# Kernel tuning notes

Hardware: AMD Instinct MI355X
Metric: run time of the kernel (lower is better)

The kernel has to match this reference:

```python
import jax, jax.numpy as jnp
import numpy as np

B, N = 4096, 12
HID = 64
SLOPE = 0.2   # GATv2Conv default negative_slope
ALPHA = 0.1   # skip-connection scale


def _gabriel_adjacency(p):
    # p: [B, N, 2] node positions. Gabriel graph: edge (i,j) iff no other
    # point k lies inside the closed disk with diameter segment (p_i, p_j).
    n = p.shape[1]
    mid = (p[:, :, None, :] + p[:, None, :, :]) * 0.5                      # [B,N,N,2]
    r2 = jnp.sum((p[:, :, None, :] - p[:, None, :, :]) ** 2, -1) * 0.25    # [B,N,N]
    d2 = jnp.sum((p[:, None, None, :, :] - mid[:, :, :, None, :]) ** 2, -1)  # [B,i,j,k]
    eye = jnp.eye(n, dtype=bool)
    excl = eye[:, None, :] | eye[None, :, :]                               # k==i or k==j
    d2 = jnp.where(excl[None], jnp.inf, d2)
    gab = jnp.all(d2 > r2[..., None], axis=-1) & (~eye)[None]
    # undirected edges + self loops (GATv2Conv add_self_loops=True default)
    return gab | jnp.swapaxes(gab, 1, 2) | eye[None]                       # [B,N,N]


def _gatv2(x, adj, wl, wr, att, b):
    # PyG GATv2Conv, heads=1: e_ij = att . leaky_relu(W_l x_j + W_r x_i),
    # alpha = softmax_j(e_ij) over neighbors, out_i = sum_j alpha_ij W_l x_j + b.
    xl = x @ wl                                                            # source feats [B,N,H]
    xr = x @ wr                                                            # target feats [B,N,H]
    s = jax.nn.leaky_relu(xl[:, None, :, :] + xr[:, :, None, :], SLOPE)    # [B,i,j,H]
    e = jnp.einsum('bijh,h->bij', s, att)
    e = jnp.where(adj, e, -1e9)
    a = jax.nn.softmax(e, axis=-1)                                         # over sources j
    return jnp.einsum('bij,bjh->bih', a, xl) + b


def _forward(batch, enc_w1, enc_b1, enc_w2, enc_b2, enc_w3, enc_b3,
             g1_wl, g1_wr, g1_att, g1_b, g2_wl, g2_wr, g2_att, g2_b,
             g3_wl, g3_wr, g3_att, g3_b, g4_wl, g4_wr, g4_att, g4_b,
             lab_w, lab_b, val_w, val_b, skip_w, skip_b):
    h = jax.nn.relu(batch @ enc_w1 + enc_b1)
    h = jax.nn.relu(h @ enc_w2 + enc_b2)
    latent = h @ enc_w3 + enc_b3                                           # [B,N,3]
    # graph construction is non-differentiable (scipy in the original)
    adj = _gabriel_adjacency(jax.lax.stop_gradient(latent[..., :2]))
    x0 = latent[..., 2:3]                                                  # [B,N,1]
    x1 = jax.nn.relu(_gatv2(x0, adj, g1_wl, g1_wr, g1_att, g1_b))
    x2 = jax.nn.relu(_gatv2(x1, adj, g2_wl, g2_wr, g2_att, g2_b))
    skip = latent @ skip_w + skip_b
    x3 = jax.nn.relu(_gatv2(x2, adj, g3_wl, g3_wr, g3_att, g3_b) + ALPHA * skip)
    logits = x3 @ lab_w + lab_b                                            # [B,N,4]
    # note: original feeds x2 (not x3) into gcn4 -- kept faithful
    x4 = jax.nn.relu(_gatv2(x2, adj, g4_wl, g4_wr, g4_att, g4_b) + ALPHA * skip)
    values = x4 @ val_w + val_b                                            # [B,N,1]
    return batch[:, :, :4], batch[:, :, 4:5], logits, values, latent


def setup_inputs():
    key = jax.random.key(0)
    ks = iter(jax.random.split(key, 40))
    def rnd(shape, s=0.1):
        return jax.random.normal(next(ks), shape, dtype=jnp.float32) * s
    inp = {"batch": jax.random.normal(next(ks), (B, N, 5), dtype=jnp.float32)}
    inp.update(enc_w1=rnd((5, HID)), enc_b1=jnp.zeros((HID,), jnp.float32),
               enc_w2=rnd((HID, HID)), enc_b2=jnp.zeros((HID,), jnp.float32),
               enc_w3=rnd((HID, 3)), enc_b3=jnp.zeros((3,), jnp.float32))
    for i, cin in zip((1, 2, 3, 4), (1, HID, HID, HID)):
        inp[f"g{i}_wl"] = rnd((cin, HID)); inp[f"g{i}_wr"] = rnd((cin, HID))
        inp[f"g{i}_att"] = rnd((HID,)); inp[f"g{i}_b"] = jnp.zeros((HID,), jnp.float32)
    inp.update(lab_w=rnd((HID, 4)), lab_b=jnp.zeros((4,), jnp.float32),
               val_w=rnd((HID, 1)), val_b=jnp.zeros((1,), jnp.float32),
               skip_w=rnd((3, HID)), skip_b=jnp.zeros((HID,), jnp.float32))
    return inp


def reference(batch, enc_w1, enc_b1, enc_w2, enc_b2, enc_w3, enc_b3,
              g1_wl, g1_wr, g1_att, g1_b, g2_wl, g2_wr, g2_att, g2_b,
              g3_wl, g3_wr, g3_att, g3_b, g4_wl, g4_wr, g4_att, g4_b,
              lab_w, lab_b, val_w, val_b, skip_w, skip_b):
    return _forward(batch, enc_w1, enc_b1, enc_w2, enc_b2, enc_w3, enc_b3,
                    g1_wl, g1_wr, g1_att, g1_b, g2_wl, g2_wr, g2_att, g2_b,
                    g3_wl, g3_wr, g3_att, g3_b, g4_wl, g4_wr, g4_att, g4_b,
                    lab_w, lab_b, val_w, val_b, skip_w, skip_b)
```

## Files before the change

kernel.cpp:

```cpp
#include <hip/hip_runtime.h>
#include <hip/hip_bf16.h>
#include <math.h>

#define N     12
#define HID   64
#define STP   68
#define XST   72
#define SLOPE 0.2f
#define ALPHA 0.1f

typedef float v2f __attribute__((ext_vector_type(2)));
typedef float v4f __attribute__((ext_vector_type(4)));
typedef int   i4  __attribute__((ext_vector_type(4)));
typedef short v8s __attribute__((ext_vector_type(8)));

static __device__ __forceinline__ v8s as_v8s(i4 v) {
    union { i4 a; v8s b; } u; u.a = v; return u.b;
}

#define OUT0 0
#define OUT1 196608
#define OUT2 245760
#define OUT3 442368
#define OUT4 491520

__global__ void prep_kernel(const float* __restrict__ enc_w2,
                            const float* __restrict__ g2_wl, const float* __restrict__ g2_wr,
                            const float* __restrict__ g3_wl, const float* __restrict__ g3_wr,
                            const float* __restrict__ g4_wl, const float* __restrict__ g4_wr,
                            const float* __restrict__ lab_w,
                            float* __restrict__ ws) {
    int t = threadIdx.x;
    int bx = blockIdx.x;
    if (bx < 64) {
        int c = bx;
        ws[t*64 + c] = enc_w2[c*64 + t];
        return;
    }
    if (bx == 112) {
        #pragma unroll
        for (int c = 0; c < 4; c++) ws[16384 + c*64 + t] = lab_w[t*4 + c];
        return;
    }
    int idx = bx - 64;
    int mat = idx >> 3, rem = idx & 7;
    int kt = rem >> 2, nt = rem & 3;
    const float* src;
    switch (mat) {
        case 0: src = g2_wl; break;
        case 1: src = g2_wr; break;
        case 2: src = g3_wl; break;
        case 3: src = g3_wr; break;
        case 4: src = g4_wl; break;
        default: src = g4_wr; break;
    }
    int quad = t >> 4, col = t & 15;
    int n = nt*16 + col;
    unsigned* dst = (unsigned*)(ws + 4096) + mat*2048 + (kt*4+nt)*256 + t*4;
    #pragma unroll
    for (int jp = 0; jp < 4; jp++) {
        int k0 = kt*32 + quad*8 + 2*jp;
        __hip_bfloat16 h0 = __float2bfloat16(src[(k0+0)*64 + n]);
        __hip_bfloat16 h1 = __float2bfloat16(src[(k0+1)*64 + n]);
        unsigned u0 = *(unsigned short*)&h0, u1 = *(unsigned short*)&h1;
        dst[jp] = u0 | (u1 << 16);
    }
}

template<bool TW>
__global__ __launch_bounds__(64, 3) void gae_kernel(
    const float* __restrict__ batch,
    const float* __restrict__ enc_w1, const float* __restrict__ enc_b1,
    const float* __restrict__ enc_w2, const float* __restrict__ enc_b2,
    const float* __restrict__ enc_w3, const float* __restrict__ enc_b3,
    const float* __restrict__ g1_wl, const float* __restrict__ g1_wr,
    const float* __restrict__ g1_att, const float* __restrict__ g1_b,
    const float* __restrict__ g2_wl, const float* __restrict__ g2_wr,
    const float* __restrict__ g2_att, const float* __restrict__ g2_b,
    const float* __restrict__ g3_wl, const float* __restrict__ g3_wr,
    const float* __restrict__ g3_att, const float* __restrict__ g3_b,
    const float* __restrict__ g4_wl, const float* __restrict__ g4_wr,
    const float* __restrict__ g4_att, const float* __restrict__ g4_b,
    const float* __restrict__ lab_w, const float* __restrict__ lab_b,
    const float* __restrict__ val_w, const float* __restrict__ val_b,
    const float* __restrict__ skip_w, const float* __restrict__ skip_b,
    const float* __restrict__ wsT,
    float* __restrict__ out)
{
    const int b = blockIdx.x;
    const int t = threadIdx.x;

    __shared__ __align__(16) float bufL[N*STP];
    __shared__ __align__(16) float bufR[N*STP];
    __shared__ __align__(16) unsigned short xB16[N*XST];
    __shared__ __align__(16) float pool[144];
    __shared__ __align__(16) float att_s[HID];
    __shared__ __align__(16) unsigned char pairs8[64];

    const v2f z2 = {0.f, 0.f};
    const v4f z4 = {0.f, 0.f, 0.f, 0.f};
    const v4f s4 = {SLOPE, SLOPE, SLOPE, SLOPE};

    const int p0 = t,        i0 = p0 / N, j0 = p0 - i0*N;
    const int p1 = t + 64,   i1 = p1 / N, j1 = p1 - i1*N;
    const int p2 = (t < 16) ? (t + 128) : 143;
    const int i2 = p2 / N,   j2 = p2 - i2*N;

    if (t < N*5) {
        float v = batch[b*(N*5) + t];
        pool[t] = v;
        int i = t / 5, f = t - i*5;
        if (f < 4) out[OUT0 + (size_t)b*(N*4) + i*4 + f] = v;
        else       out[OUT1 + (size_t)b*N + i] = v;
    }
    __syncthreads();

    {
        float acc[N];
        float bias = enc_b1[t];
        #pragma unroll
        for (int i=0;i<N;i++) acc[i] = bias;
        #pragma unroll
        for (int f=0; f<5; f++) {
            float w = enc_w1[f*HID + t];
            #pragma unroll
            for (int i=0;i<N;i++) acc[i] = fmaf(pool[i*5+f], w, acc[i]);
        }
        #pragma unroll
        for (int i=0;i<N;i++) bufL[i*STP + t] = fmaxf(acc[i], 0.f);
    }
    __syncthreads();

    {
        v2f acc[N];
        #pragma unroll
        for (int i=0;i<N;i++) acc[i] = z2;
        const float* w2p = TW ? (wsT + t*HID) : nullptr;
        for (int c=0;c<HID;c+=4) {
            v2f w01, w23;
            if (TW) {
                v4f w4 = *reinterpret_cast<const v4f*>(&w2p[c]);
                w01 = w4.xy; w23 = w4.zw;
            } else {
                w01 = (v2f){enc_w2[(c+0)*HID+t], enc_w2[(c+1)*HID+t]};
                w23 = (v2f){enc_w2[(c+2)*HID+t], enc_w2[(c+3)*HID+t]};
            }
            #pragma unroll
            for (int i=0;i<N;i++) {
                v4f xv = *reinterpret_cast<const v4f*>(&bufL[i*STP + c]);
                acc[i] = __builtin_elementwise_fma(xv.xy, w01, acc[i]);
                acc[i] = __builtin_elementwise_fma(xv.zw, w23, acc[i]);
            }
        }
        float bias = enc_b2[t];
        #pragma unroll
        for (int i=0;i<N;i++) bufR[i*STP + t] = fmaxf(bias + acc[i].x + acc[i].y, 0.f);
    }
    __syncthreads();

    if (t < N*3) {
        int i = t / 3, c = t - i*3;
        float acc = enc_b3[c];
        for (int k=0;k<HID;k+=4) {
            v4f xv = *reinterpret_cast<const v4f*>(&bufR[i*STP + k]);
            acc = fmaf(xv.x, enc_w3[(k+0)*3+c], acc);
            acc = fmaf(xv.y, enc_w3[(k+1)*3+c], acc);
            acc = fmaf(xv.z, enc_w3[(k+2)*3+c], acc);
            acc = fmaf(xv.w, enc_w3[(k+3)*3+c], acc);
        }
        pool[t] = acc;
        out[OUT4 + (size_t)b*(N*3) + t] = acc;
    }
    __syncthreads();

    float skipv[N];
    {
        float w0 = skip_w[t], w1 = skip_w[HID+t], w2 = skip_w[2*HID+t];
        float bias = skip_b[t];
        #pragma unroll
        for (int i=0;i<N;i++) {
            float v = bias;
            v = fmaf(pool[i*3+0], w0, v);
            v = fmaf(pool[i*3+1], w1, v);
            v = fmaf(pool[i*3+2], w2, v);
            skipv[i] = v;
        }
    }

    auto gab = [&](int i, int j)->bool {
        if (i == j) return false;
        float pix = pool[i*3], piy = pool[i*3+1];
        float pjx = pool[j*3], pjy = pool[j*3+1];
        float mx = (pix + pjx) * 0.5f, my = (piy + pjy) * 0.5f;
        float dx = pix - pjx, dy = piy - pjy;
        float r2 = (dx*dx + dy*dy) * 0.25f;
        bool g = true;
        #pragma unroll
        for (int k=0;k<N;k++) {
            float ex = pool[k*3] - mx, ey = pool[k*3+1] - my;
            bool ok = (k == i) || (k == j) || (ex*ex + ey*ey > r2);
            g = g && ok;
        }
        return g;
    };
    unsigned long long gb0 = __ballot(gab(i0, j0));
    unsigned long long gb1 = __ballot(gab(i1, j1));
    unsigned long long gb2 = __ballot((t < 16) && gab(i2, j2));
    auto gbit = [&](int p)->int {
        unsigned long long m = (p < 64) ? gb0 : ((p < 128) ? gb1 : gb2);
        return (int)((m >> (p & 63)) & 1ull);
    };
    const int adjA = gbit(p0) | gbit(j0*N+i0) | (i0 == j0);
    const int adjB = gbit(p1) | gbit(j1*N+i1) | (i1 == j1);
    const int adjC = (t < 16) ? (gbit(p2) | gbit(j2*N+i2) | (i2 == j2)) : 0;

    auto mbcnt64 = [&](unsigned long long m)->int {
        return __builtin_amdgcn_mbcnt_hi((unsigned)(m >> 32),
               __builtin_amdgcn_mbcnt_lo((unsigned)m, 0));
    };
    const unsigned long long am0 = __ballot(adjA != 0);
    const unsigned long long am1 = __ballot(adjB != 0);
    const unsigned long long am2 = __ballot(adjC != 0);
    const int c0  = __popcll(am0);
    const int c01 = c0 + __popcll(am1);
    const int nv  = c01 + __popcll(am2);
    const int idx0 = mbcnt64(am0);
    const int idx1 = c0  + mbcnt64(am1);
    const int idx2 = c01 + mbcnt64(am2);
    if (adjA)               pairs8[idx0] = (unsigned char)p0;
    if (adjB && idx1 < 64)  pairs8[idx1] = (unsigned char)p1;
    if (adjC && idx2 < 64)  pairs8[idx2] = (unsigned char)p2;
    const bool ovB = adjB && (idx1 >= 64);
    const bool ovC = adjC && (idx2 >= 64);
    const int nvc = nv < 64 ? nv : 64;

    auto scoreAt = [&](int i, int j)->float {
        const float* Lj = &bufL[j*STP];
        const float* Ri = &bufR[i*STP];
        v4f a = z4;
        for (int h=0; h<HID; h+=4) {
            v4f a4 = *reinterpret_cast<const v4f*>(&att_s[h]);
            v4f xl = *reinterpret_cast<const v4f*>(Lj + h);
            v4f xr = *reinterpret_cast<const v4f*>(Ri + h);
            v4f s = xl + xr;
            v4f l = __builtin_elementwise_fma(s4, __builtin_elementwise_min(s, z4),
                                              __builtin_elementwise_max(s, z4));
            a = __builtin_elementwise_fma(a4, l, a);
        }
        return (a.x + a.y) + (a.z + a.w);
    };

    auto gat_core = [&](const float* __restrict__ att, const float* __restrict__ gb,
                        int outBf16, int useSkip) {
        att_s[t] = att[t];
        pool[t] = 0.f; pool[t+64] = 0.f;
        if (t < 16) pool[t+128] = 0.f;
        __syncthreads();
        if (t < nvc) {
            int p = pairs8[t];
            int i = (p * 171) >> 11;
            int j = p - i*N;
            pool[p] = __expf(scoreAt(i, j));
        }
        if (nv > 64) {
            if (ovB) pool[p1] = __expf(scoreAt(i1, j1));
            if (ovC) pool[p2] = __expf(scoreAt(i2, j2));
        }
        __syncthreads();
        {
            float xj[N];
            #pragma unroll
            for (int j=0;j<N;j++) xj[j] = bufL[j*STP + t];
            v4f X0 = {xj[0], xj[1], xj[2],  xj[3]};
            v4f X1 = {xj[4], xj[5], xj[6],  xj[7]};
            v4f X2 = {xj[8], xj[9], xj[10], xj[11]};
            float bias = gb[t];
            #pragma unroll
            for (int i=0;i<N;i++) {
                const v4f* ep = reinterpret_cast<const v4f*>(&pool[i*N]);
                v4f e0 = ep[0], e1 = ep[1], e2 = ep[2];
                float sum = ((e0.x+e0.y)+(e0.z+e0.w))
                          + ((e1.x+e1.y)+(e1.z+e1.w))
                          + ((e2.x+e2.y)+(e2.z+e2.w));
                v4f acc = __builtin_elementwise_fma(e0, X0,
                          __builtin_elementwise_fma(e1, X1, e2*X2));
                float r = bias + ((acc.x + acc.y) + (acc.z + acc.w)) / sum;
                if (useSkip) r = fmaf(ALPHA, skipv[i], r);
                r = fmaxf(r, 0.f);
                if (outBf16) {
                    __hip_bfloat16 hv = __float2bfloat16(r);
                    xB16[i*XST + t] = *(unsigned short*)&hv;
                } else {
                    bufR[i*STP + t] = r;
                }
            }
        }
        __syncthreads();
    };

    auto stage_mfma = [&](int matL) {
        const int m = t & 15, quad = t >> 4;
        const int mc = (m < N) ? m : 0;
        i4 aF0 = *reinterpret_cast<const i4*>(&xB16[mc*XST + quad*8]);
        i4 aF1 = *reinterpret_cast<const i4*>(&xB16[mc*XST + 32 + quad*8]);
        const i4* bbase = reinterpret_cast<const i4*>(wsT + 4096);
        #pragma unroll
        for (int mm=0; mm<2; mm++) {
            const i4* bp = bbase + (matL + mm)*512;
            v4f acc[4] = {z4, z4, z4, z4};
            #pragma unroll
            for (int nt=0; nt<4; nt++) {
                i4 b0 = bp[(0*4+nt)*64 + t];
                i4 b1 = bp[(1*4+nt)*64 + t];
                acc[nt] = __builtin_amdgcn_mfma_f32_16x16x32_bf16(as_v8s(aF0), as_v8s(b0), acc[nt], 0, 0, 0);
                acc[nt] = __builtin_amdgcn_mfma_f32_16x16x32_bf16(as_v8s(aF1), as_v8s(b1), acc[nt], 0, 0, 0);
            }
            float* dst = (mm == 0) ? bufL : bufR;
            if (quad < 3) {
                #pragma unroll
                for (int nt=0; nt<4; nt++) {
                    #pragma unroll
                    for (int r=0; r<4; r++)
                        dst[(quad*4+r)*STP + nt*16 + m] = acc[nt][r];
                }
            }
        }
    };

    auto stage = [&](const float* __restrict__ wl, const float* __restrict__ wr) {
        v2f al[N], ar[N];
        #pragma unroll
        for (int i=0;i<N;i++) { al[i] = z2; ar[i] = z2; }
        for (int c=0;c<HID;c+=4) {
            v2f wl01 = (v2f){wl[(c+0)*HID+t], wl[(c+1)*HID+t]};
            v2f wl23 = (v2f){wl[(c+2)*HID+t], wl[(c+3)*HID+t]};
            v2f wr01 = (v2f){wr[(c+0)*HID+t], wr[(c+1)*HID+t]};
            v2f wr23 = (v2f){wr[(c+2)*HID+t], wr[(c+3)*HID+t]};
            #pragma unroll
            for (int i=0;i<N;i++) {
                const unsigned short* xp = &xB16[i*XST + c];
                v4f xv = { __uint_as_float((unsigned)xp[0] << 16),
                           __uint_as_float((unsigned)xp[1] << 16),
                           __uint_as_float((unsigned)xp[2] << 16),
                           __uint_as_float((unsigned)xp[3] << 16) };
                al[i] = __builtin_elementwise_fma(xv.xy, wl01, al[i]);
                al[i] = __builtin_elementwise_fma(xv.zw, wl23, al[i]);
                ar[i] = __builtin_elementwise_fma(xv.xy, wr01, ar[i]);
                ar[i] = __builtin_elementwise_fma(xv.zw, wr23, ar[i]);
            }
        }
        #pragma unroll
        for (int i=0;i<N;i++) {
            bufL[i*STP + t] = al[i].x + al[i].y;
            bufR[i*STP + t] = ar[i].x + ar[i].y;
        }
    };

    {
        float wlv = g1_wl[t], wrv = g1_wr[t];
        #pragma unroll
        for (int i=0;i<N;i++) {
            float v = pool[i*3+2];
            bufL[i*STP + t] = v * wlv;
            bufR[i*STP + t] = v * wrv;
        }
    }
    gat_core(g1_att, g1_b, 1, 0);

    if (TW) stage_mfma(0); else stage(g2_wl, g2_wr);
    gat_core(g2_att, g2_b, 1, 0);

    if (TW) stage_mfma(2); else stage(g3_wl, g3_wr);
    gat_core(g3_att, g3_b, 0, 1);

    if (t < N*4) {
        int i = t >> 2, c = t & 3;
        float acc = lab_b[c];
        if (TW) {
            const float* lwT = wsT + 16384 + c*HID;
            for (int h=0;h<HID;h+=4) {
                v4f xv = *reinterpret_cast<const v4f*>(&bufR[i*STP + h]);
                v4f w4 = *reinterpret_cast<const v4f*>(&lwT[h]);
                acc = fmaf(xv.x, w4.x, acc);
                acc = fmaf(xv.y, w4.y, acc);
                acc = fmaf(xv.z, w4.z, acc);
                acc = fmaf(xv.w, w4.w, acc);
            }
        } else {
            for (int h=0;h<HID;h+=4) {
                v4f xv = *reinterpret_cast<const v4f*>(&bufR[i*STP + h]);
                acc = fmaf(xv.x, lab_w[(h+0)*4+c], acc);
                acc = fmaf(xv.y, lab_w[(h+1)*4+c], acc);
                acc = fmaf(xv.z, lab_w[(h+2)*4+c], acc);
                acc = fmaf(xv.w, lab_w[(h+3)*4+c], acc);
            }
        }
        out[OUT2 + (size_t)b*(N*4) + t] = acc;
    }

    if (TW) stage_mfma(4); else stage(g4_wl, g4_wr);
    gat_core(g4_att, g4_b, 0, 1);

    if (t < N) {
        float acc = val_b[0];
        for (int h=0;h<HID;h+=4) {
            v4f xv = *reinterpret_cast<const v4f*>(&bufR[t*STP + h]);
            v4f w4 = *reinterpret_cast<const v4f*>(&val_w[h]);
            acc = fmaf(xv.x, w4.x, acc);
            acc = fmaf(xv.y, w4.y, acc);
            acc = fmaf(xv.z, w4.z, acc);
            acc = fmaf(xv.w, w4.w, acc);
        }
        out[OUT3 + (size_t)b*N + t] = acc;
    }
}

extern "C" void kernel_launch(void* const* d_in, const int* in_sizes, int n_in,
                              void* d_out, int out_size, void* d_ws, size_t ws_size,
                              hipStream_t stream) {
    (void)in_sizes; (void)n_in; (void)out_size;
    const bool useT = (ws_size >= (16384 + 256)*sizeof(float));
    if (useT) {
        prep_kernel<<<dim3(113), dim3(64), 0, stream>>>(
            (const float*)d_in[3],
            (const float*)d_in[11], (const float*)d_in[12],
            (const float*)d_in[15], (const float*)d_in[16],
            (const float*)d_in[19], (const float*)d_in[20],
            (const float*)d_in[23],
            (float*)d_ws);
        gae_kernel<true><<<dim3(4096), dim3(64), 0, stream>>>(
            (const float*)d_in[0],
            (const float*)d_in[1],  (const float*)d_in[2],
            (const float*)d_in[3],  (const float*)d_in[4],
            (const float*)d_in[5],  (const float*)d_in[6],
            (const float*)d_in[7],  (const float*)d_in[8],  (const float*)d_in[9],  (const float*)d_in[10],
            (const float*)d_in[11], (const float*)d_in[12], (const float*)d_in[13], (const float*)d_in[14],
            (const float*)d_in[15], (const float*)d_in[16], (const float*)d_in[17], (const float*)d_in[18],
            (const float*)d_in[19], (const float*)d_in[20], (const float*)d_in[21], (const float*)d_in[22],
            (const float*)d_in[23], (const float*)d_in[24],
            (const float*)d_in[25], (const float*)d_in[26],
            (const float*)d_in[27], (const float*)d_in[28],
            (const float*)d_ws,
            (float*)d_out);
    } else {
        gae_kernel<false><<<dim3(4096), dim3(64), 0, stream>>>(
            (const float*)d_in[0],
            (const float*)d_in[1],  (const float*)d_in[2],
            (const float*)d_in[3],  (const float*)d_in[4],
            (const float*)d_in[5],  (const float*)d_in[6],
            (const float*)d_in[7],  (const float*)d_in[8],  (const float*)d_in[9],  (const float*)d_in[10],
            (const float*)d_in[11], (const float*)d_in[12], (const float*)d_in[13], (const float*)d_in[14],
            (const float*)d_in[15], (const float*)d_in[16], (const float*)d_in[17], (const float*)d_in[18],
            (const float*)d_in[19], (const float*)d_in[20], (const float*)d_in[21], (const float*)d_in[22],
            (const float*)d_in[23], (const float*)d_in[24],
            (const float*)d_in[25], (const float*)d_in[26],
            (const float*)d_in[27], (const float*)d_in[28],
            nullptr,
            (float*)d_out);
    }
}
```

Baseline: 156.7 us.

## Store GAT stage features as bf16 in a shared LDS arena

After: 174.5 us. 1.11x slower.

```diff
diff --git a/kernel.cpp b/kernel.cpp
--- a/kernel.cpp
+++ b/kernel.cpp
@@ -16,6 +16,13 @@
 
 static __device__ __forceinline__ v8s as_v8s(i4 v) {
     union { i4 a; v8s b; } u; u.a = v; return u.b;
+}
+static __device__ __forceinline__ unsigned short f2bf(float f) {
+    __hip_bfloat16 h = __float2bfloat16(f);
+    return *(unsigned short*)&h;
+}
+static __device__ __forceinline__ float bf2f(unsigned short u) {
+    return __uint_as_float((unsigned)u << 16);
 }
 
 #define OUT0 0
@@ -32,11 +39,7 @@
                             float* __restrict__ ws) {
     int t = threadIdx.x;
     int bx = blockIdx.x;
-    if (bx < 64) {
-        int c = bx;
-        ws[t*64 + c] = enc_w2[c*64 + t];
-        return;
-    }
+    if (bx < 64) { ws[t*64 + bx] = enc_w2[bx*64 + t]; return; }
     if (bx == 112) {
         #pragma unroll
         for (int c = 0; c < 4; c++) ws[16384 + c*64 + t] = lab_w[t*4 + c];
@@ -60,10 +63,7 @@
     #pragma unroll
     for (int jp = 0; jp < 4; jp++) {
         int k0 = kt*32 + quad*8 + 2*jp;
-        __hip_bfloat16 h0 = __float2bfloat16(src[(k0+0)*64 + n]);
-        __hip_bfloat16 h1 = __float2bfloat16(src[(k0+1)*64 + n]);
-        unsigned u0 = *(unsigned short*)&h0, u1 = *(unsigned short*)&h1;
-        dst[jp] = u0 | (u1 << 16);
+        dst[jp] = (unsigned)f2bf(src[(k0+0)*64 + n]) | ((unsigned)f2bf(src[(k0+1)*64 + n]) << 16);
     }
 }
 
@@ -90,16 +90,19 @@
     const int b = blockIdx.x;
     const int t = threadIdx.x;
 
-    __shared__ __align__(16) float bufL[N*STP];
-    __shared__ __align__(16) float bufR[N*STP];
-    __shared__ __align__(16) unsigned short xB16[N*XST];
-    __shared__ __align__(16) float pool[144];
-    __shared__ __align__(16) float att_s[HID];
-    __shared__ __align__(16) unsigned char pairs8[64];
+    __shared__ __align__(16) unsigned char smem[7424];
+    float* h1 = (float*)smem;
+    float* h2 = (float*)(smem + 3264);
+    unsigned short* xl16 = (unsigned short*)smem;
+    unsigned short* xr16 = (unsigned short*)(smem + 1728);
+    unsigned short* xB16 = (unsigned short*)(smem + 3456);
+    float* pool  = (float*)(smem + 6528);
+    float* att_s = (float*)(smem + 7104);
+    unsigned char* pairs8 = smem + 7360;
 
     const v2f z2 = {0.f, 0.f};
     const v4f z4 = {0.f, 0.f, 0.f, 0.f};
-    const v4f s4 = {SLOPE, SLOPE, SLOPE, SLOPE};
+    const v2f sl2 = {SLOPE, SLOPE};
 
     const int p0 = t,        i0 = p0 / N, j0 = p0 - i0*N;
     const int p1 = t + 64,   i1 = p1 / N, j1 = p1 - i1*N;
@@ -108,26 +111,25 @@
 
     if (t < N*5) {
         float v = batch[b*(N*5) + t];
-        pool[t] = v;
         int i = t / 5, f = t - i*5;
         if (f < 4) out[OUT0 + (size_t)b*(N*4) + i*4 + f] = v;
         else       out[OUT1 + (size_t)b*N + i] = v;
     }
-    __syncthreads();
 
     {
         float acc[N];
         float bias = enc_b1[t];
         #pragma unroll
         for (int i=0;i<N;i++) acc[i] = bias;
+        const float* brow = batch + b*(N*5);
         #pragma unroll
         for (int f=0; f<5; f++) {
             float w = enc_w1[f*HID + t];
             #pragma unroll
-            for (int i=0;i<N;i++) acc[i] = fmaf(pool[i*5+f], w, acc[i]);
-        }
-        #pragma unroll
-        for (int i=0;i<N;i++) bufL[i*STP + t] = fmaxf(acc[i], 0.f);
+            for (int i=0;i<N;i++) acc[i] = fmaf(brow[i*5+f], w, acc[i]);
+        }
+        #pragma unroll
+        for (int i=0;i<N;i++) h1[i*STP + t] = fmaxf(acc[i], 0.f);
     }
     __syncthreads();
 
@@ -147,14 +149,14 @@
             }
             #pragma unroll
             for (int i=0;i<N;i++) {
-                v4f xv = *reinterpret_cast<const v4f*>(&bufL[i*STP + c]);
+                v4f xv = *reinterpret_cast<const v4f*>(&h1[i*STP + c]);
                 acc[i] = __builtin_elementwise_fma(xv.xy, w01, acc[i]);
                 acc[i] = __builtin_elementwise_fma(xv.zw, w23, acc[i]);
             }
         }
         float bias = enc_b2[t];
         #pragma unroll
-        for (int i=0;i<N;i++) bufR[i*STP + t] = fmaxf(bias + acc[i].x + acc[i].y, 0.f);
+        for (int i=0;i<N;i++) h2[i*STP + t] = fmaxf(bias + acc[i].x + acc[i].y, 0.f);
     }
     __syncthreads();
 
@@ -162,7 +164,7 @@
         int i = t / 3, c = t - i*3;
         float acc = enc_b3[c];
         for (int k=0;k<HID;k+=4) {
-            v4f xv = *reinterpret_cast<const v4f*>(&bufR[i*STP + k]);
+            v4f xv = *reinterpret_cast<const v4f*>(&h2[i*STP + k]);
             acc = fmaf(xv.x, enc_w3[(k+0)*3+c], acc);
             acc = fmaf(xv.y, enc_w3[(k+1)*3+c], acc);
             acc = fmaf(xv.z, enc_w3[(k+2)*3+c], acc);
@@ -173,18 +175,17 @@
     }
     __syncthreads();
 
+    float kx[N], ky[N], kz[N];
+    #pragma unroll
+    for (int k=0;k<N;k++) { kx[k]=pool[k*3]; ky[k]=pool[k*3+1]; kz[k]=pool[k*3+2]; }
+
     float skipv[N];
     {
         float w0 = skip_w[t], w1 = skip_w[HID+t], w2 = skip_w[2*HID+t];
         float bias = skip_b[t];
         #pragma unroll
-        for (int i=0;i<N;i++) {
-            float v = bias;
-            v = fmaf(pool[i*3+0], w0, v);
-            v = fmaf(pool[i*3+1], w1, v);
-            v = fmaf(pool[i*3+2], w2, v);
-            skipv[i] = v;
-        }
+        for (int i=0;i<N;i++)
+            skipv[i] = fmaf(kx[i], w0, fmaf(ky[i], w1, fmaf(kz[i], w2, bias)));
     }
 
     auto gab = [&](int i, int j)->bool {
@@ -197,7 +198,7 @@
         bool g = true;
         #pragma unroll
         for (int k=0;k<N;k++) {
-            float ex = pool[k*3] - mx, ey = pool[k*3+1] - my;
+            float ex = kx[k] - mx, ey = ky[k] - my;
             bool ok = (k == i) || (k == j) || (ex*ex + ey*ey > r2);
             g = g && ok;
         }
@@ -235,23 +236,31 @@
     const int nvc = nv < 64 ? nv : 64;
 
     auto scoreAt = [&](int i, int j)->float {
-        const float* Lj = &bufL[j*STP];
-        const float* Ri = &bufR[i*STP];
-        v4f a = z4;
-        for (int h=0; h<HID; h+=4) {
-            v4f a4 = *reinterpret_cast<const v4f*>(&att_s[h]);
-            v4f xl = *reinterpret_cast<const v4f*>(Lj + h);
-            v4f xr = *reinterpret_cast<const v4f*>(Ri + h);
-            v4f s = xl + xr;
-            v4f l = __builtin_elementwise_fma(s4, __builtin_elementwise_min(s, z4),
-                                              __builtin_elementwise_max(s, z4));
-            a = __builtin_elementwise_fma(a4, l, a);
-        }
-        return (a.x + a.y) + (a.z + a.w);
+        const unsigned* Lj = (const unsigned*)&xl16[j*XST];
+        const unsigned* Ri = (const unsigned*)&xr16[i*XST];
+        v2f a2 = z2;
+        for (int h=0; h<HID; h+=8) {
+            i4 lw = *reinterpret_cast<const i4*>(Lj + (h>>1));
+            i4 rw = *reinterpret_cast<const i4*>(Ri + (h>>1));
+            v4f aa = *reinterpret_cast<const v4f*>(&att_s[h]);
+            v4f ab = *reinterpret_cast<const v4f*>(&att_s[h+4]);
+            #pragma unroll
+            for (int q=0; q<4; q++) {
+                unsigned lu = (unsigned)lw[q], ru = (unsigned)rw[q];
+                v2f xl2 = { __uint_as_float(lu << 16), __uint_as_float(lu & 0xffff0000u) };
+                v2f xr2 = { __uint_as_float(ru << 16), __uint_as_float(ru & 0xffff0000u) };
+                v2f s = xl2 + xr2;
+                v2f l = __builtin_elementwise_fma(sl2, __builtin_elementwise_min(s, z2),
+                                                  __builtin_elementwise_max(s, z2));
+                v2f av = (q==0) ? aa.xy : (q==1) ? aa.zw : (q==2) ? ab.xy : ab.zw;
+                a2 = __builtin_elementwise_fma(av, l, a2);
+            }
+        }
+        return a2.x + a2.y;
     };
 
     auto gat_core = [&](const float* __restrict__ att, const float* __restrict__ gb,
-                        int outBf16, int useSkip) {
+                        unsigned short* __restrict__ out16, int useSkip) {
         att_s[t] = att[t];
         pool[t] = 0.f; pool[t+64] = 0.f;
         if (t < 16) pool[t+128] = 0.f;
@@ -270,7 +279,7 @@
         {
             float xj[N];
             #pragma unroll
-            for (int j=0;j<N;j++) xj[j] = bufL[j*STP + t];
+            for (int j=0;j<N;j++) xj[j] = bf2f(xl16[j*XST + t]);
             v4f X0 = {xj[0], xj[1], xj[2],  xj[3]};
             v4f X1 = {xj[4], xj[5], xj[6],  xj[7]};
             v4f X2 = {xj[8], xj[9], xj[10], xj[11]};
@@ -286,13 +295,7 @@
                           __builtin_elementwise_fma(e1, X1, e2*X2));
                 float r = bias + ((acc.x + acc.y) + (acc.z + acc.w)) / sum;
                 if (useSkip) r = fmaf(ALPHA, skipv[i], r);
-                r = fmaxf(r, 0.f);
-                if (outBf16) {
-                    __hip_bfloat16 hv = __float2bfloat16(r);
-                    xB16[i*XST + t] = *(unsigned short*)&hv;
-                } else {
-                    bufR[i*STP + t] = r;
-                }
+                out16[i*XST + t] = f2bf(fmaxf(r, 0.f));
             }
         }
         __syncthreads();
@@ -315,13 +318,13 @@
                 acc[nt] = __builtin_amdgcn_mfma_f32_16x16x32_bf16(as_v8s(aF0), as_v8s(b0), acc[nt], 0, 0, 0);
                 acc[nt] = __builtin_amdgcn_mfma_f32_16x16x32_bf16(as_v8s(aF1), as_v8s(b1), acc[nt], 0, 0, 0);
             }
-            float* dst = (mm == 0) ? bufL : bufR;
+            unsigned short* dst = (mm == 0) ? xl16 : xr16;
             if (quad < 3) {
                 #pragma unroll
                 for (int nt=0; nt<4; nt++) {
                     #pragma unroll
                     for (int r=0; r<4; r++)
-                        dst[(quad*4+r)*STP + nt*16 + m] = acc[nt][r];
+                        dst[(quad*4+r)*XST + nt*16 + m] = f2bf(acc[nt][r]);
                 }
             }
         }
@@ -331,28 +334,21 @@
         v2f al[N], ar[N];
         #pragma unroll
         for (int i=0;i<N;i++) { al[i] = z2; ar[i] = z2; }
-        for (int c=0;c<HID;c+=4) {
-            v2f wl01 = (v2f){wl[(c+0)*HID+t], wl[(c+1)*HID+t]};
-            v2f wl23 = (v2f){wl[(c+2)*HID+t], wl[(c+3)*HID+t]};
-            v2f wr01 = (v2f){wr[(c+0)*HID+t], wr[(c+1)*HID+t]};
-            v2f wr23 = (v2f){wr[(c+2)*HID+t], wr[(c+3)*HID+t]};
+        for (int c=0;c<HID;c+=2) {
+            v2f wlv = (v2f){wl[(c+0)*HID+t], wl[(c+1)*HID+t]};
+            v2f wrv = (v2f){wr[(c+0)*HID+t], wr[(c+1)*HID+t]};
             #pragma unroll
             for (int i=0;i<N;i++) {
-                const unsigned short* xp = &xB16[i*XST + c];
-                v4f xv = { __uint_as_float((unsigned)xp[0] << 16),
-                           __uint_as_float((unsigned)xp[1] << 16),
-                           __uint_as_float((unsigned)xp[2] << 16),
-                           __uint_as_float((unsigned)xp[3] << 16) };
-                al[i] = __builtin_elementwise_fma(xv.xy, wl01, al[i]);
-                al[i] = __builtin_elementwise_fma(xv.zw, wl23, al[i]);
-                ar[i] = __builtin_elementwise_fma(xv.xy, wr01, ar[i]);
-                ar[i] = __builtin_elementwise_fma(xv.zw, wr23, ar[i]);
+                unsigned xu = *(const unsigned*)&xB16[i*XST + c];
+                v2f xv = { __uint_as_float(xu << 16), __uint_as_float(xu & 0xffff0000u) };
+                al[i] = __builtin_elementwise_fma(xv, wlv, al[i]);
+                ar[i] = __builtin_elementwise_fma(xv, wrv, ar[i]);
             }
         }
         #pragma unroll
         for (int i=0;i<N;i++) {
-            bufL[i*STP + t] = al[i].x + al[i].y;
-            bufR[i*STP + t] = ar[i].x + ar[i].y;
+            xl16[i*XST + t] = f2bf(al[i].x + al[i].y);
+            xr16[i*XST + t] = f2bf(ar[i].x + ar[i].y);
         }
     };
 
@@ -360,56 +356,49 @@
         float wlv = g1_wl[t], wrv = g1_wr[t];
         #pragma unroll
         for (int i=0;i<N;i++) {
-            float v = pool[i*3+2];
-            bufL[i*STP + t] = v * wlv;
-            bufR[i*STP + t] = v * wrv;
-        }
-    }
-    gat_core(g1_att, g1_b, 1, 0);
+            xl16[i*XST + t] = f2bf(kz[i] * wlv);
+            xr16[i*XST + t] = f2bf(kz[i] * wrv);
+        }
+    }
+    gat_core(g1_att, g1_b, xB16, 0);
 
     if (TW) stage_mfma(0); else stage(g2_wl, g2_wr);
-    gat_core(g2_att, g2_b, 1, 0);
+    gat_core(g2_att, g2_b, xB16, 0);
 
     if (TW) stage_mfma(2); else stage(g3_wl, g3_wr);
-    gat_core(g3_att, g3_b, 0, 1);
+    gat_core(g3_att, g3_b, xr16, 1);
 
     if (t < N*4) {
         int i = t >> 2, c = t & 3;
         float acc = lab_b[c];
+        const unsigned* xp = (const unsigned*)&xr16[i*XST];
         if (TW) {
             const float* lwT = wsT + 16384 + c*HID;
-            for (int h=0;h<HID;h+=4) {
-                v4f xv = *reinterpret_cast<const v4f*>(&bufR[i*STP + h]);
-                v4f w4 = *reinterpret_cast<const v4f*>(&lwT[h]);
-                acc = fmaf(xv.x, w4.x, acc);
-                acc = fmaf(xv.y, w4.y, acc);
-                acc = fmaf(xv.z, w4.z, acc);
-                acc = fmaf(xv.w, w4.w, acc);
+            for (int h=0;h<HID;h+=2) {
+                unsigned xu = xp[h>>1];
+                acc = fmaf(__uint_as_float(xu << 16), lwT[h], acc);
+                acc = fmaf(__uint_as_float(xu & 0xffff0000u), lwT[h+1], acc);
             }
         } else {
-            for (int h=0;h<HID;h+=4) {
-                v4f xv = *reinterpret_cast<const v4f*>(&bufR[i*STP + h]);
-                acc = fmaf(xv.x, lab_w[(h+0)*4+c], acc);
-                acc = fmaf(xv.y, lab_w[(h+1)*4+c], acc);
-                acc = fmaf(xv.z, lab_w[(h+2)*4+c], acc);
-                acc = fmaf(xv.w, lab_w[(h+3)*4+c], acc);
+            for (int h=0;h<HID;h+=2) {
+                unsigned xu = xp[h>>1];
+                acc = fmaf(__uint_as_float(xu << 16), lab_w[(h+0)*4+c], acc);
+                acc = fmaf(__uint_as_float(xu & 0xffff0000u), lab_w[(h+1)*4+c], acc);
             }
         }
         out[OUT2 + (size_t)b*(N*4) + t] = acc;
     }
 
     if (TW) stage_mfma(4); else stage(g4_wl, g4_wr);
-    gat_core(g4_att, g4_b, 0, 1);
+    gat_core(g4_att, g4_b, xr16, 1);
 
     if (t < N) {
         float acc = val_b[0];
-        for (int h=0;h<HID;h+=4) {
-            v4f xv = *reinterpret_cast<const v4f*>(&bufR[t*STP + h]);
-            v4f w4 = *reinterpret_cast<const v4f*>(&val_w[h]);
-            acc = fmaf(xv.x, w4.x, acc);
-            acc = fmaf(xv.y, w4.y, acc);
-            acc = fmaf(xv.z, w4.z, acc);
-            acc = fmaf(xv.w, w4.w, acc);
+        const unsigned* xp = (const unsigned*)&xr16[t*XST];
+        for (int h=0;h<HID;h+=2) {
+            unsigned xu = xp[h>>1];
+            acc = fmaf(__uint_as_float(xu << 16), val_w[h], acc);
+            acc = fmaf(__uint_as_float(xu & 0xffff0000u), val_w[h+1], acc);
         }
         out[OUT3 + (size_t)b*N + t] = acc;
     }
```
